# Optimization experiments

Measured on AMD Instinct MI355X. Metric: run time of the kernel, lower is better.

## Reference

```python
import jax, jax.numpy as jnp
import numpy as np

PAD, SOS, EOS = 0, 1, 2
NEG = -10000.0


def _lstm(x, w_ih, w_hh, b, reverse):
    # x: [T,B,E]; torch gate order i,f,g,o; b = b_ih + b_hh combined
    T, B, _ = x.shape
    H = w_hh.shape[1]
    xg = jnp.einsum('tbe,ge->tbg', x, w_ih) + b  # precompute input gates [T,B,4H]

    def step(carry, g):
        h, c = carry
        g = g + h @ w_hh.T
        i, f, gg, o = jnp.split(g, 4, axis=-1)
        c = jax.nn.sigmoid(f) * c + jax.nn.sigmoid(i) * jnp.tanh(gg)
        h = jax.nn.sigmoid(o) * jnp.tanh(c)
        return (h, c), h

    init = (jnp.zeros((B, H), x.dtype), jnp.zeros((B, H), x.dtype))
    _, hs = jax.lax.scan(step, init, xg, reverse=reverse)
    return hs  # [T,B,H]


def setup_inputs() -> dict:
    key = jax.random.key(0)
    T, B, V, E, H, K = 256, 64, 50000, 512, 512, 24
    ks = jax.random.split(key, 12)
    xw = jax.random.randint(ks[0], (T, B), 4, V)
    y_tags = jax.random.randint(ks[1], (T, B), 3, K)  # real tags, > EOS so mask is all ones
    y0 = jnp.concatenate([jnp.full((1, B), SOS, dtype=y_tags.dtype), y_tags], axis=0)  # [T+1,B]
    s = lambda k, sh: (jax.random.normal(k, sh, jnp.float32) * 0.02)
    emb = s(ks[2], (V, E))
    w_ih_f = s(ks[3], (4 * H, E)); w_hh_f = s(ks[4], (4 * H, H)); b_f = jnp.zeros((4 * H,), jnp.float32)
    w_ih_b = s(ks[5], (4 * H, E)); w_hh_b = s(ks[6], (4 * H, H)); b_b = jnp.zeros((4 * H,), jnp.float32)
    w_out = s(ks[7], (K, 2 * H)); b_out = jnp.zeros((K,), jnp.float32)
    trans = jax.random.normal(ks[8], (K, K), jnp.float32)
    trans = trans.at[SOS, :].set(NEG).at[:, EOS].set(NEG).at[:, PAD].set(NEG).at[PAD, :].set(NEG)
    trans = trans.at[PAD, EOS].set(0.0).at[PAD, PAD].set(0.0)
    return dict(xw=xw, y0=y0, emb=emb, w_ih_f=w_ih_f, w_hh_f=w_hh_f, b_f=b_f,
                w_ih_b=w_ih_b, w_hh_b=w_hh_b, b_b=b_b, w_out=w_out, b_out=b_out, trans=trans)


def reference(xw, y0, emb, w_ih_f, w_hh_f, b_f, w_ih_b, w_hh_b, b_b, w_out, b_out, trans):
    mask = (y0[1:] > PAD).astype(emb.dtype)  # [T,B]
    x = emb[xw]  # [T,B,E]
    hf = _lstm(x, w_ih_f, w_hh_f, b_f, reverse=False)
    hb = _lstm(x, w_ih_b, w_hh_b, b_b, reverse=True)
    h = jnp.concatenate([hf, hb], axis=-1) @ w_out.T + b_out  # [T,B,K]
    h = h * mask[:, :, None]
    B, K = h.shape[1], h.shape[2]

    # --- CRF partition function (forward algorithm) ---
    score0 = jnp.full((B, K), NEG, h.dtype).at[:, SOS].set(0.0)

    def step(score, inp):
        ht, mt = inp  # ht: [B,K], mt: [B]
        # new[b,j] = logsumexp_i(score[b,i] + ht[b,j] + trans[j,i])
        new = jax.nn.logsumexp(score[:, None, :] + ht[:, :, None] + trans[None, :, :], axis=2)
        return new * mt[:, None] + score * (1.0 - mt[:, None]), None

    score, _ = jax.lax.scan(step, score0, (h, mask))
    Z = jax.nn.logsumexp(score + trans[EOS], axis=1)  # [B]

    # --- gold path score ---
    emit = jnp.take_along_axis(h, y0[1:][:, :, None], axis=2)[..., 0]  # [T,B]
    tr = trans[y0[1:], y0[:-1]]  # [T,B]
    lens = mask.sum(0).astype(jnp.int32)  # [B]
    last = jnp.take_along_axis(y0, lens[None, :], axis=0)[0]  # y0[lens[b], b]
    gold = ((emit + tr) * mask).sum(0) + trans[EOS, last]  # [B]

    return jnp.mean(Z - gold)
```

## Files before the change

### kernel.cpp

```cpp
#include <hip/hip_runtime.h>

typedef __attribute__((ext_vector_type(8))) short short8;
typedef __attribute__((ext_vector_type(4))) float f32x4;

#define NEGV -10000.0f

__device__ __forceinline__ float bfu2f(unsigned short u) {
  unsigned int x = ((unsigned int)u) << 16;
  return __builtin_bit_cast(float, x);
}
__device__ __forceinline__ unsigned short f2bfu(float f) {
  unsigned int x = __builtin_bit_cast(unsigned int, f);
  x += 0x7fffu + ((x >> 16) & 1u);
  return (unsigned short)(x >> 16);
}
__device__ __forceinline__ float fsig(float x) {
  return 1.0f / (1.0f + __expf(-x));
}
__device__ __forceinline__ float ftanh(float x) {
  x = fminf(15.0f, fmaxf(-15.0f, x));
  float e = __expf(-2.0f * x);
  return (1.0f - e) / (1.0f + e);
}

__global__ __launch_bounds__(256) void prep_kernel(
    const float* __restrict__ wihf, const float* __restrict__ wihb,
    const float* __restrict__ whhf, const float* __restrict__ whhb,
    const float* __restrict__ wo, const float* __restrict__ bfv,
    const float* __restrict__ bbv,
    unsigned short* __restrict__ wih_c, unsigned short* __restrict__ whh_c,
    unsigned short* __restrict__ wout_c, float* __restrict__ bias_c) {
  size_t i = (size_t)blockIdx.x * 256 + threadIdx.x;
  const size_t n_half = 2048u * 512u;
  const size_t n_wih = 2u * n_half;
  const size_t n_wo = 24u * 1024u;
  if (i < n_wih) {
    float v = (i < n_half) ? wihf[i] : wihb[i - n_half];
    wih_c[i] = f2bfu(v);
  } else if (i < 2u * n_wih) {
    size_t j = i - n_wih;
    float v = (j < n_half) ? whhf[j] : whhb[j - n_half];
    whh_c[j] = f2bfu(v);
  } else if (i < 2u * n_wih + n_wo) {
    size_t j = i - 2u * n_wih;
    wout_c[j] = f2bfu(wo[j]);
  } else if (i < 2u * n_wih + n_wo + 4096u) {
    size_t j = i - 2u * n_wih - n_wo;
    bias_c[j] = (j < 2048u) ? bfv[j] : bbv[j - 2048u];
  }
}

__global__ __launch_bounds__(256) void gemm_xg_kernel(
    const int* __restrict__ xw,
    const float* __restrict__ emb,
    const unsigned short* __restrict__ Bm,
    const float* __restrict__ bias,
    unsigned short* __restrict__ C) {
  __shared__ alignas(16) char As[16384];
  __shared__ alignas(16) char Bs[16384];
  int m0 = blockIdx.x * 128, n0 = blockIdx.y * 128;
  int tid = threadIdx.x;
  int wv = tid >> 6, l = tid & 63;
  int wm = wv >> 1, wn = wv & 1;
  int col = l & 15, quad = l >> 4;
  int tok[4];
#pragma unroll
  for (int q = 0; q < 4; ++q) tok[q] = xw[m0 + ((q * 4096 + tid * 16) >> 7)];
  f32x4 zero4 = {0.f, 0.f, 0.f, 0.f};
  f32x4 acc[4][4];
#pragma unroll
  for (int i = 0; i < 4; ++i)
#pragma unroll
    for (int j = 0; j < 4; ++j) acc[i][j] = zero4;
  for (int kt = 0; kt < 8; ++kt) {
#pragma unroll
    for (int q = 0; q < 4; ++q) {
      int o = q * 4096 + tid * 16;
      int row = o >> 7;
      int cb = o & 127;
      int swz = cb ^ ((row & 7) << 4);
      const float* sa = emb + (size_t)tok[q] * 512 + kt * 64 + (cb >> 1);
      f32x4 f0 = *(const f32x4*)sa;
      f32x4 f1 = *(const f32x4*)(sa + 4);
      short8 va;
#pragma unroll
      for (int j = 0; j < 4; ++j) {
        va[j] = (short)f2bfu(f0[j]);
        va[4 + j] = (short)f2bfu(f1[j]);
      }
      *(short8*)(As + row * 128 + swz) = va;
      short8 vb = *(const short8*)(Bm + (size_t)(n0 + row) * 512 + kt * 64 + (cb >> 1));
      *(short8*)(Bs + row * 128 + swz) = vb;
    }
    __syncthreads();
#pragma unroll
    for (int kk = 0; kk < 2; ++kk) {
      short8 af[4], bf8[4];
#pragma unroll
      for (int mi = 0; mi < 4; ++mi) {
        int r = wm * 64 + mi * 16 + col;
        int cb = kk * 64 + quad * 16;
        af[mi] = *(const short8*)(As + r * 128 + (cb ^ ((r & 7) << 4)));
      }
#pragma unroll
      for (int ni = 0; ni < 4; ++ni) {
        int r = wn * 64 + ni * 16 + col;
        int cb = kk * 64 + quad * 16;
        bf8[ni] = *(const short8*)(Bs + r * 128 + (cb ^ ((r & 7) << 4)));
      }
#pragma unroll
      for (int mi = 0; mi < 4; ++mi)
#pragma unroll
        for (int ni = 0; ni < 4; ++ni)
          acc[mi][ni] = __builtin_amdgcn_mfma_f32_16x16x32_bf16(af[mi], bf8[ni], acc[mi][ni], 0, 0, 0);
    }
    __syncthreads();
  }
#pragma unroll
  for (int ni = 0; ni < 4; ++ni) {
    int cg = n0 + wn * 64 + ni * 16 + col;
    float bv = bias[cg];
#pragma unroll
    for (int mi = 0; mi < 4; ++mi) {
#pragma unroll
      for (int r = 0; r < 4; ++r) {
        int rg = m0 + wm * 64 + mi * 16 + quad * 4 + r;
        C[(size_t)rg * 4096 + cg] = f2bfu(acc[mi][ni][r] + bv);
      }
    }
  }
}

__global__ __launch_bounds__(64, 1) void scan_kernel(
    const unsigned short* __restrict__ whh,
    const unsigned short* __restrict__ xg,
    unsigned short* __restrict__ hfp,
    unsigned short* __restrict__ hbp) {
  __shared__ alignas(16) unsigned short tbuf[128];
  int wid = blockIdx.x;
  int l = threadIdx.x;
  int dir = wid & 1;
  int g = (wid >> 1) & 63;
  int wv = (wid >> 7) & 3;
  int u0 = g * 8;
  int col = l & 15, quad = l >> 4;
  int b_row = wv * 16 + quad * 4;
  short8 bfr[2][16];
#pragma unroll
  for (int n = 0; n < 2; ++n) {
    int blk = n * 2 + (col >> 3);
    int gr = blk * 512 + u0 + (col & 7);
    const char* base = (const char*)(whh + ((size_t)dir * 2048 + gr) * 512 + quad * 8);
#pragma unroll
    for (int kk = 0; kk < 16; ++kk)
      asm volatile("global_load_dwordx4 %0, %1, off" : "=v"(bfr[n][kk]) : "v"(base + kk * 64));
  }
  asm volatile("s_waitcnt vmcnt(0)" ::: "memory");
  unsigned short* hseq = dir ? hbp : hfp;
  float cst[4] = {0.f, 0.f, 0.f, 0.f};
  f32x4 zero4 = {0.f, 0.f, 0.f, 0.f};
  for (int s = 0; s < 256; ++s) {
    int t = dir ? (255 - s) : s;
    float xgv[2][4];
#pragma unroll
    for (int n = 0; n < 2; ++n) {
      int gc = dir * 2048 + (n * 2 + (col >> 3)) * 512 + u0 + (col & 7);
#pragma unroll
      for (int r = 0; r < 4; ++r)
        xgv[n][r] = bfu2f(xg[((size_t)t * 64 + b_row + r) * 4096 + gc]);
    }
    f32x4 a0 = zero4, a1 = zero4;
    if (s > 0) {
      int tprev = dir ? (t + 1) : (t - 1);
      const char* pbase = (const char*)hseq + (size_t)tprev * 65536 + quad * 1024 +
                          (wv * 16 + col) * 16;
      short8 af[16];
      unsigned long long bal;
      do {
#pragma unroll
        for (int kk = 0; kk < 16; ++kk)
          asm volatile("global_load_dwordx4 %0, %1, off sc0 sc1" : "=v"(af[kk]) : "v"(pbase + kk * 4096));
        asm volatile("s_waitcnt vmcnt(0)" ::: "memory");
        unsigned int anystale = 0u;
#pragma unroll
        for (int kk = 0; kk < 16; ++kk)
          anystale |= (((unsigned short)af[kk][0]) == 0xFFFFu) ? 1u : 0u;
        bal = __ballot(anystale != 0u);
      } while (bal != 0ull);
      __builtin_amdgcn_sched_barrier(0);
#pragma unroll
      for (int kk = 0; kk < 16; ++kk) {
        a0 = __builtin_amdgcn_mfma_f32_16x16x32_bf16(af[kk], bfr[0][kk], a0, 0, 0, 0);
        a1 = __builtin_amdgcn_mfma_f32_16x16x32_bf16(af[kk], bfr[1][kk], a1, 0, 0, 0);
      }
    }
    {
      bool low = (col < 8);
#pragma unroll
      for (int r = 0; r < 4; ++r) {
        float g0 = a0[r] + xgv[0][r];
        float g1 = a1[r] + xgv[1][r];
        float p0 = __shfl_xor(g0, 8);
        float p1 = __shfl_xor(g1, 8);
        float iv = low ? g0 : p0;
        float fv = low ? p0 : g0;
        float gv = low ? g1 : p1;
        float ov = low ? p1 : g1;
        float cn = fsig(fv) * cst[r] + fsig(iv) * ftanh(gv);
        cst[r] = cn;
        float hv = fsig(ov) * ftanh(cn);
        if (low) tbuf[(quad * 4 + r) * 8 + (col & 7)] = f2bfu(hv);
      }
    }
    asm volatile("s_waitcnt lgkmcnt(0)" ::: "memory");
    if (l < 16) {
      short8 hrow = *(const short8*)(tbuf + l * 8);
      char* dst = (char*)hseq + (size_t)t * 65536 + g * 1024 + (wv * 16 + l) * 16;
      asm volatile("global_store_dwordx4 %0, %1, off sc0 sc1" :: "v"(dst), "v"(hrow) : "memory");
    }
  }
}

__global__ __launch_bounds__(256) void logits_kernel(
    const unsigned short* __restrict__ hfp, const unsigned short* __restrict__ hbp,
    const unsigned short* __restrict__ wout, const float* __restrict__ bout,
    const int* __restrict__ y0, float* __restrict__ lg) {
  int t = blockIdx.x;
  int w = threadIdx.x >> 6, l = threadIdx.x & 63;
  int nt = w & 1, mh = w >> 1;
  int col = l & 15, quad = l >> 4;
  int wr = nt * 16 + col;
  if (wr > 23) wr = 23;
  short8 bw[32];
#pragma unroll
  for (int kk = 0; kk < 32; ++kk)
    bw[kk] = *(const short8*)(wout + (size_t)wr * 1024 + kk * 32 + quad * 8);
  f32x4 zero4 = {0.f, 0.f, 0.f, 0.f};
  const char* pf = (const char*)hfp + (size_t)t * 65536;
  const char* pb = (const char*)hbp + (size_t)t * 65536;
#pragma unroll
  for (int mt = 0; mt < 2; ++mt) {
    int b0 = mh * 32 + mt * 16;
    f32x4 acc = zero4;
#pragma unroll
    for (int kk = 0; kk < 16; ++kk) {
      short8 a = *(const short8*)(pf + (kk * 4 + quad) * 1024 + (b0 + col) * 16);
      acc = __builtin_amdgcn_mfma_f32_16x16x32_bf16(a, bw[kk], acc, 0, 0, 0);
    }
#pragma unroll
    for (int kk = 0; kk < 16; ++kk) {
      short8 a = *(const short8*)(pb + (kk * 4 + quad) * 1024 + (b0 + col) * 16);
      acc = __builtin_amdgcn_mfma_f32_16x16x32_bf16(a, bw[16 + kk], acc, 0, 0, 0);
    }
    int ko = nt * 16 + col;
    if (ko < 24) {
      float bv = bout[ko];
#pragma unroll
      for (int r = 0; r < 4; ++r) {
        int b = b0 + quad * 4 + r;
        float mk = (y0[(t + 1) * 64 + b] > 0) ? 1.f : 0.f;
        lg[((size_t)t * 64 + b) * 32 + ko] = mk * (acc[r] + bv);
      }
    }
  }
}

__global__ __launch_bounds__(64) void crf_kernel(
    const float* __restrict__ lg, const int* __restrict__ y0,
    const float* __restrict__ trans, float* __restrict__ res) {
  int b = blockIdx.x, l = threadIdx.x;
  __shared__ float tl[600];
  __shared__ float sc[24];
  for (int i = l; i < 576; i += 64) tl[(i / 24) * 25 + (i % 24)] = trans[i];
  if (l < 24) sc[l] = (l == 1) ? 0.f : NEGV;
  __syncthreads();
  float gold = 0.f;
  int lens = 0;
  for (int t = l; t < 256; t += 64) {
    int y1 = y0[(t + 1) * 64 + b];
    int yp = y0[t * 64 + b];
    if (y1 > 0) {
      gold += lg[((size_t)t * 64 + b) * 32 + y1] + tl[y1 * 25 + yp];
      lens += 1;
    }
  }
#pragma unroll
  for (int off = 32; off > 0; off >>= 1) {
    gold += __shfl_down(gold, off);
    lens += __shfl_down(lens, off);
  }
  gold = __shfl(gold, 0);
  lens = __shfl(lens, 0);
  int last = y0[lens * 64 + b];
  gold += tl[2 * 25 + last];
  int lc = (l < 24) ? l : 23;
  float trow[24];
#pragma unroll
  for (int j = 0; j < 24; ++j) trow[j] = tl[lc * 25 + j];
  for (int t = 0; t < 256; ++t) {
    int y1 = y0[(t + 1) * 64 + b];
    if (y1 > 0) {
      float ns = 0.f;
      if (l < 24) {
        float ht = lg[((size_t)t * 64 + b) * 32 + l];
        float mx = -3.0e38f;
        float sj[24];
#pragma unroll
        for (int j = 0; j < 24; ++j) {
          sj[j] = sc[j] + trow[j];
          mx = fmaxf(mx, sj[j]);
        }
        float sm = 0.f;
#pragma unroll
        for (int j = 0; j < 24; ++j) sm += __expf(sj[j] - mx);
        ns = ht + mx + __logf(sm);
      }
      __syncthreads();
      if (l < 24) sc[l] = ns;
      __syncthreads();
    }
  }
  float v = (l < 24) ? sc[l] + tl[2 * 25 + l] : -3.0e38f;
  float mx = v;
#pragma unroll
  for (int off = 32; off > 0; off >>= 1) mx = fmaxf(mx, __shfl_xor(mx, off));
  float se = (l < 24) ? __expf(v - mx) : 0.f;
#pragma unroll
  for (int off = 32; off > 0; off >>= 1) se += __shfl_xor(se, off);
  float Z = mx + __logf(se);
  if (l == 0) res[b] = Z - gold;
}

__global__ __launch_bounds__(64) void reduce_kernel(const float* __restrict__ res,
                                                    float* __restrict__ out) {
  int l = threadIdx.x;
  float v = res[l];
#pragma unroll
  for (int off = 32; off > 0; off >>= 1) v += __shfl_down(v, off);
  if (l == 0) out[0] = v * (1.0f / 64.0f);
}

extern "C" void kernel_launch(void* const* d_in, const int* in_sizes, int n_in,
                              void* d_out, int out_size, void* d_ws, size_t ws_size,
                              hipStream_t stream) {
  (void)in_sizes; (void)n_in; (void)out_size; (void)ws_size;
  const int* xw = (const int*)d_in[0];
  const int* y0 = (const int*)d_in[1];
  const float* emb = (const float*)d_in[2];
  const float* wihf = (const float*)d_in[3];
  const float* whhf = (const float*)d_in[4];
  const float* bfv = (const float*)d_in[5];
  const float* wihb = (const float*)d_in[6];
  const float* whhb = (const float*)d_in[7];
  const float* bbv = (const float*)d_in[8];
  const float* wo = (const float*)d_in[9];
  const float* bo = (const float*)d_in[10];
  const float* tr = (const float*)d_in[11];
  char* ws = (char*)d_ws;
  unsigned short* xg = (unsigned short*)(ws + 0);
  unsigned short* wih_c = (unsigned short*)(ws + 150994944);
  unsigned short* whh_c = (unsigned short*)(ws + 155189248);
  unsigned short* wout_c = (unsigned short*)(ws + 159383552);
  float* bias_c = (float*)(ws + 159432704);
  unsigned short* hfp = (unsigned short*)(ws + 159449088);
  unsigned short* hbp = (unsigned short*)(ws + 176226304);
  float* lg = (float*)(ws + 193003520);
  float* res = (float*)(ws + 195104768);

  hipMemsetAsync(hfp, 0xFF, 16777216, stream);
  hipMemsetAsync(hbp, 0xFF, 16777216, stream);
  prep_kernel<<<16496, 256, 0, stream>>>(wihf, wihb, whhf, whhb, wo, bfv, bbv,
                                         wih_c, whh_c, wout_c, bias_c);
  gemm_xg_kernel<<<dim3(128, 32), 256, 0, stream>>>(xw, emb, wih_c, bias_c, xg);
  scan_kernel<<<512, 64, 0, stream>>>(whh_c, xg, hfp, hbp);
  logits_kernel<<<256, 256, 0, stream>>>(hfp, hbp, wout_c, bo, y0, lg);
  crf_kernel<<<64, 64, 0, stream>>>(lg, y0, tr, res);
  reduce_kernel<<<1, 64, 0, stream>>>(res, (float*)d_out);
}
```

Measured before the change: 1.183 ms.

## Pre-gather embeddings to bf16 and use direct global-to-LDS loads in input GEMM

The embedding gather and fp32-to-bf16 conversion move into the prep kernel, which writes a contiguous bf16 activation matrix. The input-gate GEMM then streams both operands with global_load_lds, applying the swizzle on the source address instead of in registers. This is meant to stop each n-block from re-gathering and re-converting fp32 embedding rows, and to cut register staging. In exchange it adds an extra pass over 16MB of workspace and a larger prep launch.

```diff
diff --git a/kernel.cpp b/kernel.cpp
--- a/kernel.cpp
+++ b/kernel.cpp
@@ -27,13 +27,16 @@
     const float* __restrict__ wihf, const float* __restrict__ wihb,
     const float* __restrict__ whhf, const float* __restrict__ whhb,
     const float* __restrict__ wo, const float* __restrict__ bfv,
-    const float* __restrict__ bbv,
+    const float* __restrict__ bbv, const int* __restrict__ xw,
+    const float* __restrict__ emb,
     unsigned short* __restrict__ wih_c, unsigned short* __restrict__ whh_c,
-    unsigned short* __restrict__ wout_c, float* __restrict__ bias_c) {
+    unsigned short* __restrict__ wout_c, float* __restrict__ bias_c,
+    unsigned short* __restrict__ xbf) {
   size_t i = (size_t)blockIdx.x * 256 + threadIdx.x;
   const size_t n_half = 2048u * 512u;
   const size_t n_wih = 2u * n_half;
   const size_t n_wo = 24u * 1024u;
+  const size_t TOT = 2u * n_wih + n_wo + 4096u;
   if (i < n_wih) {
     float v = (i < n_half) ? wihf[i] : wihb[i - n_half];
     wih_c[i] = f2bfu(v);
@@ -44,15 +47,18 @@
   } else if (i < 2u * n_wih + n_wo) {
     size_t j = i - 2u * n_wih;
     wout_c[j] = f2bfu(wo[j]);
-  } else if (i < 2u * n_wih + n_wo + 4096u) {
+  } else if (i < TOT) {
     size_t j = i - 2u * n_wih - n_wo;
     bias_c[j] = (j < 2048u) ? bfv[j] : bbv[j - 2048u];
+  } else if (i < TOT + 8388608u) {
+    size_t j = i - TOT;
+    int tb = (int)(j >> 9), e = (int)(j & 511u);
+    xbf[j] = f2bfu(emb[(size_t)xw[tb] * 512 + e]);
   }
 }
 
 __global__ __launch_bounds__(256) void gemm_xg_kernel(
-    const int* __restrict__ xw,
-    const float* __restrict__ emb,
+    const unsigned short* __restrict__ A,
     const unsigned short* __restrict__ Bm,
     const float* __restrict__ bias,
     unsigned short* __restrict__ C) {
@@ -63,9 +69,16 @@
   int wv = tid >> 6, l = tid & 63;
   int wm = wv >> 1, wn = wv & 1;
   int col = l & 15, quad = l >> 4;
-  int tok[4];
-#pragma unroll
-  for (int q = 0; q < 4; ++q) tok[q] = xw[m0 + ((q * 4096 + tid * 16) >> 7)];
+  int src_off[4], lbase[4];
+#pragma unroll
+  for (int q = 0; q < 4; ++q) {
+    int o = q * 4096 + tid * 16;
+    int row = o >> 7, p = o & 127;
+    src_off[q] = row * 1024 + (p ^ ((row & 7) << 4));
+    lbase[q] = q * 4096 + wv * 1024;
+  }
+  const char* abase = (const char*)A + (size_t)m0 * 1024;
+  const char* bbase = (const char*)Bm + (size_t)n0 * 1024;
   f32x4 zero4 = {0.f, 0.f, 0.f, 0.f};
   f32x4 acc[4][4];
 #pragma unroll
@@ -75,22 +88,12 @@
   for (int kt = 0; kt < 8; ++kt) {
 #pragma unroll
     for (int q = 0; q < 4; ++q) {
-      int o = q * 4096 + tid * 16;
-      int row = o >> 7;
-      int cb = o & 127;
-      int swz = cb ^ ((row & 7) << 4);
-      const float* sa = emb + (size_t)tok[q] * 512 + kt * 64 + (cb >> 1);
-      f32x4 f0 = *(const f32x4*)sa;
-      f32x4 f1 = *(const f32x4*)(sa + 4);
-      short8 va;
-#pragma unroll
-      for (int j = 0; j < 4; ++j) {
-        va[j] = (short)f2bfu(f0[j]);
-        va[4 + j] = (short)f2bfu(f1[j]);
-      }
-      *(short8*)(As + row * 128 + swz) = va;
-      short8 vb = *(const short8*)(Bm + (size_t)(n0 + row) * 512 + kt * 64 + (cb >> 1));
-      *(short8*)(Bs + row * 128 + swz) = vb;
+      __builtin_amdgcn_global_load_lds(
+          (const __attribute__((address_space(1))) void*)(abase + src_off[q] + kt * 128),
+          (__attribute__((address_space(3))) void*)(As + lbase[q]), 16, 0, 0);
+      __builtin_amdgcn_global_load_lds(
+          (const __attribute__((address_space(1))) void*)(bbase + src_off[q] + kt * 128),
+          (__attribute__((address_space(3))) void*)(Bs + lbase[q]), 16, 0, 0);
     }
     __syncthreads();
 #pragma unroll
@@ -358,6 +361,7 @@
   const float* tr = (const float*)d_in[11];
   char* ws = (char*)d_ws;
   unsigned short* xg = (unsigned short*)(ws + 0);
+  unsigned short* xbf = (unsigned short*)(ws + 134217728);
   unsigned short* wih_c = (unsigned short*)(ws + 150994944);
   unsigned short* whh_c = (unsigned short*)(ws + 155189248);
   unsigned short* wout_c = (unsigned short*)(ws + 159383552);
@@ -369,9 +373,9 @@
 
   hipMemsetAsync(hfp, 0xFF, 16777216, stream);
   hipMemsetAsync(hbp, 0xFF, 16777216, stream);
-  prep_kernel<<<16496, 256, 0, stream>>>(wihf, wihb, whhf, whhb, wo, bfv, bbv,
-                                         wih_c, whh_c, wout_c, bias_c);
-  gemm_xg_kernel<<<dim3(128, 32), 256, 0, stream>>>(xw, emb, wih_c, bias_c, xg);
+  prep_kernel<<<49264, 256, 0, stream>>>(wihf, wihb, whhf, whhb, wo, bfv, bbv,
+                                         xw, emb, wih_c, whh_c, wout_c, bias_c, xbf);
+  gemm_xg_kernel<<<dim3(128, 32), 256, 0, stream>>>(xbf, wih_c, bias_c, xg);
   scan_kernel<<<512, 64, 0, stream>>>(whh_c, xg, hfp, hbp);
   logits_kernel<<<256, 256, 0, stream>>>(hfp, hbp, wout_c, bo, y0, lg);
   crf_kernel<<<64, 64, 0, stream>>>(lg, y0, tr, res);
```

New measurement: 1.176 ms (median of 2 runs). No clear change (-0.6%).
